# Performance work log

Measured on AMD Instinct MI355X. Metric: run time of the kernel, lower is better.

The kernel has to match this reference:

```python
import jax, jax.numpy as jnp
import numpy as np

N = 50000      # nodes
E = 400000     # edges (before self-loops)
NFEAT = 256
NHID = 64
NHEAD = 8
NOUT = 128


def gat_conv(h, src, dst, W, attn_l, attn_r, bias, n, H, D):
    """DGL GATConv (eval mode: feat_drop/attn_drop are no-ops), negative_slope=0.2."""
    feat = (h @ W).reshape(n, H, D)                      # [N,H,D]
    el = jnp.einsum('nhd,hd->nh', feat, attn_l)          # [N,H]
    er = jnp.einsum('nhd,hd->nh', feat, attn_r)          # [N,H]
    e = jax.nn.leaky_relu(el[src] + er[dst], 0.2)        # [E,H]
    # segment softmax over incoming edges of each dst node
    m = jax.ops.segment_max(e, dst, num_segments=n)      # [N,H] (every node has a self-loop)
    ex = jnp.exp(e - m[dst])
    denom = jax.ops.segment_sum(ex, dst, num_segments=n)
    a = ex / denom[dst]                                  # [E,H]
    rst = jax.ops.segment_sum(a[:, :, None] * feat[src], dst, num_segments=n)  # [N,H,D]
    return rst + bias.reshape(1, H, D)


def setup_inputs() -> dict:
    key = jax.random.key(0)
    ks = jax.random.split(key, 10)
    s = 0.1
    x = jax.random.normal(ks[0], (N, NFEAT), jnp.float32)
    edge_index = jax.random.randint(ks[1], (2, E), 0, N, dtype=jnp.int64)
    W1 = jax.random.normal(ks[2], (NFEAT, NHEAD * NHID), jnp.float32) * s
    al1 = jax.random.normal(ks[3], (NHEAD, NHID), jnp.float32) * s
    ar1 = jax.random.normal(ks[4], (NHEAD, NHID), jnp.float32) * s
    b1 = jax.random.normal(ks[5], (NHEAD * NHID,), jnp.float32) * s
    W2 = jax.random.normal(ks[6], (NHEAD * NHID, NOUT), jnp.float32) * s
    al2 = jax.random.normal(ks[7], (1, NOUT), jnp.float32) * s
    ar2 = jax.random.normal(ks[8], (1, NOUT), jnp.float32) * s
    b2 = jax.random.normal(ks[9], (NOUT,), jnp.float32) * s
    return {"x": x, "edge_index": edge_index, "W1": W1, "al1": al1, "ar1": ar1,
            "b1": b1, "W2": W2, "al2": al2, "ar2": ar2, "b2": b2}


def reference(x, edge_index, W1, al1, ar1, b1, W2, al2, ar2, b2):
    n = x.shape[0]
    loop = jnp.arange(n, dtype=edge_index.dtype)
    src = jnp.concatenate([edge_index[0], loop])  # dgl.add_self_loop
    dst = jnp.concatenate([edge_index[1], loop])
    # hidden layer (dropout is identity in eval mode)
    h = gat_conv(x, src, dst, W1, al1, ar1, b1, n, NHEAD, NHID).reshape(n, NFEAT * 2)
    h = jax.nn.elu(h)
    out = gat_conv(h, src, dst, W2, al2, ar2, b2, n, 1, NOUT).reshape(n, NOUT)
    return out
```

## Files before the change

### kernel.cpp

```cpp
#include <hip/hip_runtime.h>

#define NFEAT 256
#define NHID 64
#define NHEAD 8
#define HID1 512
#define NOUT 128

typedef unsigned short ushort_t;
typedef unsigned int uint_t;
typedef __attribute__((ext_vector_type(8))) short short8;
typedef __attribute__((ext_vector_type(4))) float floatx4;
typedef __attribute__((ext_vector_type(4))) ushort_t ushort4_t;

static __device__ __forceinline__ float bf2f(uint_t s) {
    return __uint_as_float(s << 16);
}
static __device__ __forceinline__ ushort_t f2bf(float f) {
    uint_t u = __float_as_uint(f);
    u += 0x7FFF + ((u >> 16) & 1);
    return (ushort_t)(u >> 16);
}

__global__ void k_hist(const int* __restrict__ dstA, int E, int n, int* __restrict__ deg) {
    int i = blockIdx.x * blockDim.x + threadIdx.x;
    if (i >= E + n) return;
    int d = (i < E) ? dstA[i] : (i - E);
    atomicAdd(&deg[d], 1);
}

__global__ __launch_bounds__(1024) void k_scan(const int* __restrict__ deg, int* __restrict__ indptr, int n) {
    __shared__ int part[1024];
    int t = threadIdx.x;
    int chunk = (n + 1023) >> 10;
    int b = t * chunk;
    int e = min(b + chunk, n);
    int s = 0;
    for (int i = b; i < e; ++i) s += deg[i];
    part[t] = s;
    __syncthreads();
    for (int off = 1; off < 1024; off <<= 1) {
        int v = (t >= off) ? part[t - off] : 0;
        __syncthreads();
        part[t] += v;
        __syncthreads();
    }
    int run = (t == 0) ? 0 : part[t - 1];
    for (int i = b; i < e; ++i) { indptr[i] = run; run += deg[i]; }
    if (t == 1023) indptr[n] = part[1023];
}

__global__ void k_fill(const int* __restrict__ srcA, const int* __restrict__ dstA, int E, int n,
                       const int* __restrict__ indptr, int* __restrict__ cnt, int* __restrict__ csr_src) {
    int i = blockIdx.x * blockDim.x + threadIdx.x;
    if (i >= E + n) return;
    int s, d;
    if (i < E) { s = srcA[i]; d = dstA[i]; } else { s = i - E; d = s; }
    int pos = indptr[d] + atomicAdd(&cnt[d], 1);
    csr_src[pos] = s;
}

__global__ void k_cast(const float* __restrict__ x, ushort_t* __restrict__ xb, int total4) {
    int i = blockIdx.x * blockDim.x + threadIdx.x;
    if (i >= total4) return;
    floatx4 f = ((const floatx4*)x)[i];
    ushort4_t o;
    #pragma unroll
    for (int j = 0; j < 4; ++j) o[j] = f2bf(f[j]);
    ((ushort4_t*)xb)[i] = o;
}

__global__ void k_prepw(const float* __restrict__ W, ushort_t* __restrict__ Wt, int K, int N) {
    int i = blockIdx.x * blockDim.x + threadIdx.x;
    if (i >= K * N) return;
    int nn = i / K, kk = i % K;
    Wt[i] = f2bf(W[(size_t)kk * N + nn]);
}

__global__ __launch_bounds__(256) void k_gemm128(const ushort_t* __restrict__ A,
                                                 const ushort_t* __restrict__ Bt,
                                                 ushort_t* __restrict__ C,
                                                 int M, int N, int K) {
    __shared__ __align__(16) ushort_t As[128 * 32];
    __shared__ __align__(16) ushort_t Bs[128 * 32];
    const int t = threadIdx.x;
    const int w = t >> 6, lane = t & 63;
    const int l16 = lane & 15, quad = lane >> 4;
    const int m0 = blockIdx.y * 128, n0 = blockIdx.x * 128;
    const int r0 = (w >> 1) * 64;
    const int c0 = (w & 1) * 64;

    floatx4 acc[4][4] = {};

    const int srow[2] = { (0 * 256 + t) >> 2, (1 * 256 + t) >> 2 };
    const int skp = (t & 3) * 8;
    const int wbase0 = (0 * 256 + (t & ~63)) * 8;
    const int wbase1 = (1 * 256 + (t & ~63)) * 8;

    for (int k0 = 0; k0 < K; k0 += 32) {
        {
            int gr0 = m0 + srow[0]; if (gr0 >= M) gr0 = M - 1;
            int gr1 = m0 + srow[1]; if (gr1 >= M) gr1 = M - 1;
            const ushort_t* gpa0 = A + (size_t)gr0 * K + k0 + skp;
            const ushort_t* gpa1 = A + (size_t)gr1 * K + k0 + skp;
            const ushort_t* gpb0 = Bt + (size_t)(n0 + srow[0]) * K + k0 + skp;
            const ushort_t* gpb1 = Bt + (size_t)(n0 + srow[1]) * K + k0 + skp;
            __builtin_amdgcn_global_load_lds((const __attribute__((address_space(1))) void*)gpa0,
                (__attribute__((address_space(3))) void*)(As + wbase0), 16, 0, 0);
            __builtin_amdgcn_global_load_lds((const __attribute__((address_space(1))) void*)gpa1,
                (__attribute__((address_space(3))) void*)(As + wbase1), 16, 0, 0);
            __builtin_amdgcn_global_load_lds((const __attribute__((address_space(1))) void*)gpb0,
                (__attribute__((address_space(3))) void*)(Bs + wbase0), 16, 0, 0);
            __builtin_amdgcn_global_load_lds((const __attribute__((address_space(1))) void*)gpb1,
                (__attribute__((address_space(3))) void*)(Bs + wbase1), 16, 0, 0);
        }
        __syncthreads();

        short8 af[4], bf[4];
        #pragma unroll
        for (int i = 0; i < 4; ++i)
            af[i] = *(const short8*)(As + (r0 + i * 16 + l16) * 32 + quad * 8);
        #pragma unroll
        for (int j = 0; j < 4; ++j)
            bf[j] = *(const short8*)(Bs + (c0 + j * 16 + l16) * 32 + quad * 8);
        #pragma unroll
        for (int i = 0; i < 4; ++i)
            #pragma unroll
            for (int j = 0; j < 4; ++j)
                acc[i][j] = __builtin_amdgcn_mfma_f32_16x16x32_bf16(af[i], bf[j], acc[i][j], 0, 0, 0);
        __syncthreads();
    }

    #pragma unroll
    for (int i = 0; i < 4; ++i) {
        #pragma unroll
        for (int r = 0; r < 4; ++r) {
            int row = m0 + r0 + i * 16 + quad * 4 + r;
            if (row < M) {
                #pragma unroll
                for (int j = 0; j < 4; ++j)
                    C[(size_t)row * N + n0 + c0 + j * 16 + l16] = f2bf(acc[i][j][r]);
            }
        }
    }
}

__global__ __launch_bounds__(256) void k_elr1(const uint_t* __restrict__ fb, const float* __restrict__ al,
                                              const float* __restrict__ ar, float* __restrict__ el,
                                              float* __restrict__ er, int n) {
    int node = blockIdx.x;
    int t = threadIdx.x;
    uint_t u = fb[(size_t)node * 256 + t];
    float lo = bf2f(u & 0xFFFF), hi = bf2f(u >> 16);
    float p = lo * al[2 * t] + hi * al[2 * t + 1];
    float q = lo * ar[2 * t] + hi * ar[2 * t + 1];
    for (int o = 16; o > 0; o >>= 1) {
        p += __shfl_down(p, o, 32);
        q += __shfl_down(q, o, 32);
    }
    if ((t & 31) == 0) {
        int h = t >> 5;
        el[node * NHEAD + h] = p;
        er[node * NHEAD + h] = q;
    }
}

__global__ __launch_bounds__(256) void k_agg1(const uint_t* __restrict__ fb, const float* __restrict__ el,
                                              const float* __restrict__ er, const float* __restrict__ b1,
                                              const int* __restrict__ indptr, const int* __restrict__ csr_src,
                                              uint_t* __restrict__ h1b, int n) {
    int node = blockIdx.x;
    int t = threadIdx.x;
    int h = t >> 5;
    float erv = er[node * NHEAD + h];
    int e0 = indptr[node], e1 = indptr[node + 1];
    float a0 = 0.f, a1 = 0.f, den = 0.f;
    int e = e0;
    for (; e + 1 < e1; e += 2) {
        int s0 = csr_src[e], s1 = csr_src[e + 1];
        float x0 = el[s0 * NHEAD + h] + erv;
        float x1 = el[s1 * NHEAD + h] + erv;
        uint_t u0 = fb[(size_t)s0 * 256 + t];
        uint_t u1 = fb[(size_t)s1 * 256 + t];
        x0 = (x0 > 0.f) ? x0 : 0.2f * x0;
        x1 = (x1 > 0.f) ? x1 : 0.2f * x1;
        float w0 = __expf(x0), w1 = __expf(x1);
        den += w0 + w1;
        a0 += w0 * bf2f(u0 & 0xFFFF) + w1 * bf2f(u1 & 0xFFFF);
        a1 += w0 * bf2f(u0 >> 16) + w1 * bf2f(u1 >> 16);
    }
    if (e < e1) {
        int s = csr_src[e];
        float x = el[s * NHEAD + h] + erv;
        x = (x > 0.f) ? x : 0.2f * x;
        float w = __expf(x);
        den += w;
        uint_t u = fb[(size_t)s * 256 + t];
        a0 += w * bf2f(u & 0xFFFF);
        a1 += w * bf2f(u >> 16);
    }
    float inv = 1.f / den;
    float v0 = a0 * inv + b1[2 * t];
    float v1 = a1 * inv + b1[2 * t + 1];
    v0 = (v0 > 0.f) ? v0 : (__expf(v0) - 1.f);
    v1 = (v1 > 0.f) ? v1 : (__expf(v1) - 1.f);
    h1b[(size_t)node * 256 + t] = (uint_t)f2bf(v0) | ((uint_t)f2bf(v1) << 16);
}

__global__ __launch_bounds__(256) void k_elr2(const uint_t* __restrict__ fb2, const float* __restrict__ al2,
                                              const float* __restrict__ ar2, float* __restrict__ el2,
                                              float* __restrict__ er2, int n) {
    int wid = blockIdx.x * 4 + (threadIdx.x >> 6);
    int lane = threadIdx.x & 63;
    if (wid >= n) return;
    uint_t u = fb2[(size_t)wid * 64 + lane];
    float lo = bf2f(u & 0xFFFF), hi = bf2f(u >> 16);
    float p = lo * al2[2 * lane] + hi * al2[2 * lane + 1];
    float q = lo * ar2[2 * lane] + hi * ar2[2 * lane + 1];
    for (int o = 32; o > 0; o >>= 1) { p += __shfl_down(p, o); q += __shfl_down(q, o); }
    if (lane == 0) { el2[wid] = p; er2[wid] = q; }
}

__global__ __launch_bounds__(256) void k_agg2(const uint_t* __restrict__ fb2, const float* __restrict__ el2,
                                              const float* __restrict__ er2, const float* __restrict__ b2,
                                              const int* __restrict__ indptr, const int* __restrict__ csr_src,
                                              float* __restrict__ out, int n) {
    int wid = blockIdx.x * 4 + (threadIdx.x >> 6);
    int lane = threadIdx.x & 63;
    if (wid >= n) return;
    float erv = er2[wid];
    int e0 = indptr[wid], e1 = indptr[wid + 1];
    float a0 = 0.f, a1 = 0.f, den = 0.f;
    int e = e0;
    for (; e + 1 < e1; e += 2) {
        int s0 = csr_src[e], s1 = csr_src[e + 1];
        float x0 = el2[s0] + erv;
        float x1 = el2[s1] + erv;
        uint_t u0 = fb2[(size_t)s0 * 64 + lane];
        uint_t u1 = fb2[(size_t)s1 * 64 + lane];
        x0 = (x0 > 0.f) ? x0 : 0.2f * x0;
        x1 = (x1 > 0.f) ? x1 : 0.2f * x1;
        float w0 = __expf(x0), w1 = __expf(x1);
        den += w0 + w1;
        a0 += w0 * bf2f(u0 & 0xFFFF) + w1 * bf2f(u1 & 0xFFFF);
        a1 += w0 * bf2f(u0 >> 16) + w1 * bf2f(u1 >> 16);
    }
    if (e < e1) {
        int s = csr_src[e];
        float x = el2[s] + erv;
        x = (x > 0.f) ? x : 0.2f * x;
        float w = __expf(x);
        den += w;
        uint_t u = fb2[(size_t)s * 64 + lane];
        a0 += w * bf2f(u & 0xFFFF);
        a1 += w * bf2f(u >> 16);
    }
    float inv = 1.f / den;
    float2 o;
    o.x = a0 * inv + b2[2 * lane];
    o.y = a1 * inv + b2[2 * lane + 1];
    ((float2*)out)[(size_t)wid * 64 + lane] = o;
}

extern "C" void kernel_launch(void* const* d_in, const int* in_sizes, int n_in,
                              void* d_out, int out_size, void* d_ws, size_t ws_size,
                              hipStream_t stream) {
    const float* x   = (const float*)d_in[0];
    const int*   ei  = (const int*)d_in[1];
    const float* W1  = (const float*)d_in[2];
    const float* al1 = (const float*)d_in[3];
    const float* ar1 = (const float*)d_in[4];
    const float* b1  = (const float*)d_in[5];
    const float* W2  = (const float*)d_in[6];
    const float* al2 = (const float*)d_in[7];
    const float* ar2 = (const float*)d_in[8];
    const float* b2  = (const float*)d_in[9];

    const int n  = in_sizes[0] / NFEAT;
    const int E  = in_sizes[1] / 2;
    const int ET = E + n;
    const int* srcA = ei;
    const int* dstA = ei + E;

    char* ws = (char*)d_ws;
    size_t off = 0;
    auto alloc = [&](size_t bytes) -> void* {
        void* p = ws + off;
        off += (bytes + 255) & ~(size_t)255;
        return p;
    };
    ushort_t* xb     = (ushort_t*)alloc((size_t)n * NFEAT * 2);
    ushort_t* feat1b = (ushort_t*)alloc((size_t)n * HID1 * 2);
    ushort_t* h1b    = (ushort_t*)alloc((size_t)n * HID1 * 2);
    ushort_t* feat2b = (ushort_t*)alloc((size_t)n * NOUT * 2);
    ushort_t* W1t    = (ushort_t*)alloc((size_t)NFEAT * HID1 * 2);
    ushort_t* W2t    = (ushort_t*)alloc((size_t)HID1 * NOUT * 2);
    float* el1 = (float*)alloc((size_t)n * NHEAD * 4);
    float* er1 = (float*)alloc((size_t)n * NHEAD * 4);
    float* el2 = (float*)alloc((size_t)n * 4);
    float* er2 = (float*)alloc((size_t)n * 4);
    int* indptr = (int*)alloc((size_t)(n + 1) * 4);
    int* deg    = (int*)alloc((size_t)n * 4);
    int* cnt    = (int*)alloc((size_t)n * 4);
    int* csr    = (int*)alloc((size_t)ET * 4);

    hipMemsetAsync(deg, 0, (size_t)n * 4, stream);
    hipMemsetAsync(cnt, 0, (size_t)n * 4, stream);

    k_hist<<<(ET + 255) / 256, 256, 0, stream>>>(dstA, E, n, deg);
    k_scan<<<1, 1024, 0, stream>>>(deg, indptr, n);
    k_fill<<<(ET + 255) / 256, 256, 0, stream>>>(srcA, dstA, E, n, indptr, cnt, csr);

    k_cast<<<((n * NFEAT / 4) + 255) / 256, 256, 0, stream>>>(x, xb, n * NFEAT / 4);
    k_prepw<<<(NFEAT * HID1 + 255) / 256, 256, 0, stream>>>(W1, W1t, NFEAT, HID1);
    k_prepw<<<(HID1 * NOUT + 255) / 256, 256, 0, stream>>>(W2, W2t, HID1, NOUT);

    k_gemm128<<<dim3(HID1 / 128, (n + 127) / 128), 256, 0, stream>>>(xb, W1t, feat1b, n, HID1, NFEAT);
    k_elr1<<<n, 256, 0, stream>>>((const uint_t*)feat1b, al1, ar1, el1, er1, n);
    k_agg1<<<n, 256, 0, stream>>>((const uint_t*)feat1b, el1, er1, b1, indptr, csr, (uint_t*)h1b, n);

    k_gemm128<<<dim3(NOUT / 128, (n + 127) / 128), 256, 0, stream>>>(h1b, W2t, feat2b, n, NOUT, HID1);
    k_elr2<<<(n + 3) / 4, 256, 0, stream>>>((const uint_t*)feat2b, al2, ar2, el2, er2, n);
    k_agg2<<<(n + 3) / 4, 256, 0, stream>>>((const uint_t*)feat2b, el2, er2, b2, indptr, csr, (float*)d_out, n);
}
```

Measured before the change: 451.6 us.

## Precompute per-edge attention weights in separate kernels and unroll aggregation by four

Adds a CSR destination array and two edge-parallel kernels that compute exp(leaky_relu(el[src]+er[dst])) once per edge and head and store them. The aggregation kernels then read these precomputed weights instead of gathering el and computing exp redundantly across the 32 lanes of each head. The edge loop is also unrolled from two to four to put more gathers in flight. The cost is two extra launches, an extra csr_dst write, and the extra memory traffic of writing and reading the weight arrays (about 14 MB for layer 1).

```diff
diff --git a/kernel.cpp b/kernel.cpp
--- a/kernel.cpp
+++ b/kernel.cpp
@@ -50,13 +50,15 @@
 }
 
 __global__ void k_fill(const int* __restrict__ srcA, const int* __restrict__ dstA, int E, int n,
-                       const int* __restrict__ indptr, int* __restrict__ cnt, int* __restrict__ csr_src) {
+                       const int* __restrict__ indptr, int* __restrict__ cnt,
+                       int* __restrict__ csr_src, int* __restrict__ csr_dst) {
     int i = blockIdx.x * blockDim.x + threadIdx.x;
     if (i >= E + n) return;
     int s, d;
     if (i < E) { s = srcA[i]; d = dstA[i]; } else { s = i - E; d = s; }
     int pos = indptr[d] + atomicAdd(&cnt[d], 1);
     csr_src[pos] = s;
+    csr_dst[pos] = d;
 }
 
 __global__ void k_cast(const float* __restrict__ x, ushort_t* __restrict__ xb, int total4) {
@@ -164,37 +166,60 @@
     }
 }
 
-__global__ __launch_bounds__(256) void k_agg1(const uint_t* __restrict__ fb, const float* __restrict__ el,
-                                              const float* __restrict__ er, const float* __restrict__ b1,
+__global__ void k_wgt1(const int* __restrict__ csr_src, const int* __restrict__ csr_dst,
+                       const float* __restrict__ el, const float* __restrict__ er,
+                       float* __restrict__ wcsr, int ET) {
+    int idx = blockIdx.x * blockDim.x + threadIdx.x;
+    if (idx >= ET * NHEAD) return;
+    int e = idx >> 3, h = idx & 7;
+    int s = csr_src[e], d = csr_dst[e];
+    float x = el[s * NHEAD + h] + er[d * NHEAD + h];
+    x = (x > 0.f) ? x : 0.2f * x;
+    wcsr[idx] = __expf(x);
+}
+
+__global__ void k_wgt2(const int* __restrict__ csr_src, const int* __restrict__ csr_dst,
+                       const float* __restrict__ el2, const float* __restrict__ er2,
+                       float* __restrict__ wcsr, int ET) {
+    int e = blockIdx.x * blockDim.x + threadIdx.x;
+    if (e >= ET) return;
+    int s = csr_src[e], d = csr_dst[e];
+    float x = el2[s] + er2[d];
+    x = (x > 0.f) ? x : 0.2f * x;
+    wcsr[e] = __expf(x);
+}
+
+__global__ __launch_bounds__(256) void k_agg1(const uint_t* __restrict__ fb, const float* __restrict__ wcsr,
+                                              const float* __restrict__ b1,
                                               const int* __restrict__ indptr, const int* __restrict__ csr_src,
                                               uint_t* __restrict__ h1b, int n) {
     int node = blockIdx.x;
     int t = threadIdx.x;
     int h = t >> 5;
-    float erv = er[node * NHEAD + h];
     int e0 = indptr[node], e1 = indptr[node + 1];
     float a0 = 0.f, a1 = 0.f, den = 0.f;
     int e = e0;
-    for (; e + 1 < e1; e += 2) {
-        int s0 = csr_src[e], s1 = csr_src[e + 1];
-        float x0 = el[s0 * NHEAD + h] + erv;
-        float x1 = el[s1 * NHEAD + h] + erv;
+    for (; e + 3 < e1; e += 4) {
+        int s0 = csr_src[e], s1 = csr_src[e + 1], s2 = csr_src[e + 2], s3 = csr_src[e + 3];
+        float w0 = wcsr[(size_t)e * NHEAD + h];
+        float w1 = wcsr[(size_t)(e + 1) * NHEAD + h];
+        float w2 = wcsr[(size_t)(e + 2) * NHEAD + h];
+        float w3 = wcsr[(size_t)(e + 3) * NHEAD + h];
         uint_t u0 = fb[(size_t)s0 * 256 + t];
         uint_t u1 = fb[(size_t)s1 * 256 + t];
-        x0 = (x0 > 0.f) ? x0 : 0.2f * x0;
-        x1 = (x1 > 0.f) ? x1 : 0.2f * x1;
-        float w0 = __expf(x0), w1 = __expf(x1);
-        den += w0 + w1;
-        a0 += w0 * bf2f(u0 & 0xFFFF) + w1 * bf2f(u1 & 0xFFFF);
-        a1 += w0 * bf2f(u0 >> 16) + w1 * bf2f(u1 >> 16);
-    }
-    if (e < e1) {
+        uint_t u2 = fb[(size_t)s2 * 256 + t];
+        uint_t u3 = fb[(size_t)s3 * 256 + t];
+        den += (w0 + w1) + (w2 + w3);
+        a0 += w0 * bf2f(u0 & 0xFFFF) + w1 * bf2f(u1 & 0xFFFF)
+            + w2 * bf2f(u2 & 0xFFFF) + w3 * bf2f(u3 & 0xFFFF);
+        a1 += w0 * bf2f(u0 >> 16) + w1 * bf2f(u1 >> 16)
+            + w2 * bf2f(u2 >> 16) + w3 * bf2f(u3 >> 16);
+    }
+    for (; e < e1; ++e) {
         int s = csr_src[e];
-        float x = el[s * NHEAD + h] + erv;
-        x = (x > 0.f) ? x : 0.2f * x;
-        float w = __expf(x);
+        float w = wcsr[(size_t)e * NHEAD + h];
+        uint_t u = fb[(size_t)s * 256 + t];
         den += w;
-        uint_t u = fb[(size_t)s * 256 + t];
         a0 += w * bf2f(u & 0xFFFF);
         a1 += w * bf2f(u >> 16);
     }
@@ -220,37 +245,34 @@
     if (lane == 0) { el2[wid] = p; er2[wid] = q; }
 }
 
-__global__ __launch_bounds__(256) void k_agg2(const uint_t* __restrict__ fb2, const float* __restrict__ el2,
-                                              const float* __restrict__ er2, const float* __restrict__ b2,
+__global__ __launch_bounds__(256) void k_agg2(const uint_t* __restrict__ fb2, const float* __restrict__ wcsr,
+                                              const float* __restrict__ b2,
                                               const int* __restrict__ indptr, const int* __restrict__ csr_src,
                                               float* __restrict__ out, int n) {
     int wid = blockIdx.x * 4 + (threadIdx.x >> 6);
     int lane = threadIdx.x & 63;
     if (wid >= n) return;
-    float erv = er2[wid];
     int e0 = indptr[wid], e1 = indptr[wid + 1];
     float a0 = 0.f, a1 = 0.f, den = 0.f;
     int e = e0;
-    for (; e + 1 < e1; e += 2) {
-        int s0 = csr_src[e], s1 = csr_src[e + 1];
-        float x0 = el2[s0] + erv;
-        float x1 = el2[s1] + erv;
+    for (; e + 3 < e1; e += 4) {
+        int s0 = csr_src[e], s1 = csr_src[e + 1], s2 = csr_src[e + 2], s3 = csr_src[e + 3];
+        float w0 = wcsr[e], w1 = wcsr[e + 1], w2 = wcsr[e + 2], w3 = wcsr[e + 3];
         uint_t u0 = fb2[(size_t)s0 * 64 + lane];
         uint_t u1 = fb2[(size_t)s1 * 64 + lane];
-        x0 = (x0 > 0.f) ? x0 : 0.2f * x0;
-        x1 = (x1 > 0.f) ? x1 : 0.2f * x1;
-        float w0 = __expf(x0), w1 = __expf(x1);
-        den += w0 + w1;
-        a0 += w0 * bf2f(u0 & 0xFFFF) + w1 * bf2f(u1 & 0xFFFF);
-        a1 += w0 * bf2f(u0 >> 16) + w1 * bf2f(u1 >> 16);
-    }
-    if (e < e1) {
+        uint_t u2 = fb2[(size_t)s2 * 64 + lane];
+        uint_t u3 = fb2[(size_t)s3 * 64 + lane];
+        den += (w0 + w1) + (w2 + w3);
+        a0 += w0 * bf2f(u0 & 0xFFFF) + w1 * bf2f(u1 & 0xFFFF)
+            + w2 * bf2f(u2 & 0xFFFF) + w3 * bf2f(u3 & 0xFFFF);
+        a1 += w0 * bf2f(u0 >> 16) + w1 * bf2f(u1 >> 16)
+            + w2 * bf2f(u2 >> 16) + w3 * bf2f(u3 >> 16);
+    }
+    for (; e < e1; ++e) {
         int s = csr_src[e];
-        float x = el2[s] + erv;
-        x = (x > 0.f) ? x : 0.2f * x;
-        float w = __expf(x);
+        float w = wcsr[e];
+        uint_t u = fb2[(size_t)s * 64 + lane];
         den += w;
-        uint_t u = fb2[(size_t)s * 64 + lane];
         a0 += w * bf2f(u & 0xFFFF);
         a1 += w * bf2f(u >> 16);
     }
@@ -298,17 +320,20 @@
     float* er1 = (float*)alloc((size_t)n * NHEAD * 4);
     float* el2 = (float*)alloc((size_t)n * 4);
     float* er2 = (float*)alloc((size_t)n * 4);
-    int* indptr = (int*)alloc((size_t)(n + 1) * 4);
-    int* deg    = (int*)alloc((size_t)n * 4);
-    int* cnt    = (int*)alloc((size_t)n * 4);
-    int* csr    = (int*)alloc((size_t)ET * 4);
+    float* wcsr1 = (float*)alloc((size_t)ET * NHEAD * 4);
+    float* wcsr2 = (float*)alloc((size_t)ET * 4);
+    int* indptr  = (int*)alloc((size_t)(n + 1) * 4);
+    int* deg     = (int*)alloc((size_t)n * 4);
+    int* cnt     = (int*)alloc((size_t)n * 4);
+    int* csr     = (int*)alloc((size_t)ET * 4);
+    int* csrd    = (int*)alloc((size_t)ET * 4);
 
     hipMemsetAsync(deg, 0, (size_t)n * 4, stream);
     hipMemsetAsync(cnt, 0, (size_t)n * 4, stream);
 
     k_hist<<<(ET + 255) / 256, 256, 0, stream>>>(dstA, E, n, deg);
     k_scan<<<1, 1024, 0, stream>>>(deg, indptr, n);
-    k_fill<<<(ET + 255) / 256, 256, 0, stream>>>(srcA, dstA, E, n, indptr, cnt, csr);
+    k_fill<<<(ET + 255) / 256, 256, 0, stream>>>(srcA, dstA, E, n, indptr, cnt, csr, csrd);
 
     k_cast<<<((n * NFEAT / 4) + 255) / 256, 256, 0, stream>>>(x, xb, n * NFEAT / 4);
     k_prepw<<<(NFEAT * HID1 + 255) / 256, 256, 0, stream>>>(W1, W1t, NFEAT, HID1);
@@ -316,9 +341,11 @@
 
     k_gemm128<<<dim3(HID1 / 128, (n + 127) / 128), 256, 0, stream>>>(xb, W1t, feat1b, n, HID1, NFEAT);
     k_elr1<<<n, 256, 0, stream>>>((const uint_t*)feat1b, al1, ar1, el1, er1, n);
-    k_agg1<<<n, 256, 0, stream>>>((const uint_t*)feat1b, el1, er1, b1, indptr, csr, (uint_t*)h1b, n);
+    k_wgt1<<<(ET * NHEAD + 255) / 256, 256, 0, stream>>>(csr, csrd, el1, er1, wcsr1, ET);
+    k_agg1<<<n, 256, 0, stream>>>((const uint_t*)feat1b, wcsr1, b1, indptr, csr, (uint_t*)h1b, n);
 
     k_gemm128<<<dim3(NOUT / 128, (n + 127) / 128), 256, 0, stream>>>(h1b, W2t, feat2b, n, NOUT, HID1);
     k_elr2<<<(n + 3) / 4, 256, 0, stream>>>((const uint_t*)feat2b, al2, ar2, el2, er2, n);
-    k_agg2<<<(n + 3) / 4, 256, 0, stream>>>((const uint_t*)feat2b, el2, er2, b2, indptr, csr, (float*)d_out, n);
-}
+    k_wgt2<<<(ET + 255) / 256, 256, 0, stream>>>(csr, csrd, el2, er2, wcsr2, ET);
+    k_agg2<<<(n + 3) / 4, 256, 0, stream>>>((const uint_t*)feat2b, wcsr2, b2, indptr, csr, (float*)d_out, n);
+}
```

Measured after the change: 442.6 us. 2.0% less time.
